# Kernel tuning notes

Measured on AMD Instinct MI355X. Metric: run time of the kernel, lower is better.

Reference implementation:

```python
import jax, jax.numpy as jnp
import numpy as np

NUM_HEADS = 8
LN_EPS = 1e-5


def layer_norm(x, g, b):
    m = jnp.mean(x, axis=-1, keepdims=True)
    v = jnp.mean((x - m) ** 2, axis=-1, keepdims=True)
    return (x - m) * jax.lax.rsqrt(v + LN_EPS) * g + b


def setup_inputs() -> dict:
    key = jax.random.key(0)
    B, Nq, Nk, D = 4, 2048, 2048, 256
    F = 4 * D
    ks = jax.random.split(key, 12)
    s = 0.02
    inp = {
        "q": jax.random.normal(ks[0], (B, Nq, D), jnp.float32),
        "x": jax.random.normal(ks[1], (B, Nk, D), jnp.float32),
        "Wq": jax.random.normal(ks[2], (D, D), jnp.float32) * s,
        "bq": jnp.zeros((D,), jnp.float32),
        "Wk": jax.random.normal(ks[3], (D, D), jnp.float32) * s,
        "bk": jnp.zeros((D,), jnp.float32),
        "Wv": jax.random.normal(ks[4], (D, D), jnp.float32) * s,
        "bv": jnp.zeros((D,), jnp.float32),
        "Wo": jax.random.normal(ks[5], (D, D), jnp.float32) * s,
        "bo": jnp.zeros((D,), jnp.float32),
        "Wm": jax.random.normal(ks[6], (D, F), jnp.float32) * s,
        "bm": jnp.zeros((F,), jnp.float32),
        "We": jax.random.normal(ks[7], (F, D), jnp.float32) * s,
        "be": jnp.zeros((D,), jnp.float32),
        "g0": jnp.ones((D,), jnp.float32),
        "b0": jnp.zeros((D,), jnp.float32),
        "g1": jnp.ones((D,), jnp.float32),
        "b1": jnp.zeros((D,), jnp.float32),
    }
    return inp


def reference(q, x, Wq, bq, Wk, bk, Wv, bv, Wo, bo, Wm, bm, We, be, g0, b0, g1, b1):
    B, Nq, D = q.shape
    H = NUM_HEADS
    dh = D // H
    scale = 1.0 / np.sqrt(dh).astype(np.float32)
    # projections, split into heads (split(dim_split,2)+cat(.,0) == head reshape)
    Q = (q @ Wq + bq).reshape(B, Nq, H, dh)
    K = (x @ Wk + bk).reshape(B, -1, H, dh)
    V = (x @ Wv + bv).reshape(B, -1, H, dh)
    A = jax.nn.softmax(jnp.einsum("bqhd,bkhd->bhqk", Q, K) * scale, axis=-1)
    # residual on the projected query (Q_ + A @ V_), merge heads
    O = (Q + jnp.einsum("bhqk,bkhd->bqhd", A, V)).reshape(B, Nq, D)
    O = layer_norm(O, g0, b0)
    O = O + jax.nn.relu(O @ Wo + bo)
    identity = O
    O = layer_norm(O, g1, b1)  # dropout p=0.0 is identity
    O = jax.nn.relu(O @ Wm + bm) @ We + be
    return O + identity
```

## Files before the change

### kernel.cpp

```cpp
#include <hip/hip_runtime.h>
#include <math.h>
#include <stdint.h>

typedef __attribute__((ext_vector_type(8))) __bf16 bf16x8;
typedef __attribute__((ext_vector_type(16))) float f32x16;

#define Z16 {0.f,0.f,0.f,0.f,0.f,0.f,0.f,0.f,0.f,0.f,0.f,0.f,0.f,0.f,0.f,0.f}

__device__ __forceinline__ unsigned short f2b(float f) {
  union { float f; uint32_t u; } v; v.f = f;
  uint32_t r = (v.u + 0x7FFFu + ((v.u >> 16) & 1u)) >> 16;
  return (unsigned short)r;
}
__device__ __forceinline__ float b2f(unsigned short u) {
  union { uint32_t u; float f; } v; v.u = ((uint32_t)u) << 16;
  return v.f;
}
__device__ __forceinline__ uint32_t pk2(float a, float b) {
  return (uint32_t)f2b(a) | ((uint32_t)f2b(b) << 16);
}
__device__ __forceinline__ uint32_t cvtpk(float lo, float hi) {
  uint32_t r;
  asm("v_cvt_pk_bf16_f32 %0, %1, %2" : "=v"(r) : "v"(lo), "v"(hi));
  return r;
}
__device__ __forceinline__ void glds16(const void* g, void* l) {
  __builtin_amdgcn_global_load_lds(
      (const __attribute__((address_space(1))) void*)g,
      (__attribute__((address_space(3))) void*)l, 16, 0, 0);
}
#define MFMA32(a, b, c) __builtin_amdgcn_mfma_f32_32x32x16_bf16(a, b, c, 0, 0, 0)

__global__ __launch_bounds__(256) void prep(
    const float* __restrict__ q, const float* __restrict__ x,
    unsigned short* __restrict__ qh, unsigned short* __restrict__ xh,
    const float* __restrict__ Wq, const float* __restrict__ Wk,
    const float* __restrict__ Wv, const float* __restrict__ Wo,
    const float* __restrict__ Wm, const float* __restrict__ We,
    unsigned short* __restrict__ WqT, unsigned short* __restrict__ WkvT,
    unsigned short* __restrict__ WoT, unsigned short* __restrict__ WmT,
    unsigned short* __restrict__ WeT,
    const float* __restrict__ bk, const float* __restrict__ bv,
    float* __restrict__ bkv) {
  __shared__ float T[64][68];
  const int bx = blockIdx.x, tid = threadIdx.x;
  if (bx < 2048) {
    const float* src = (bx < 1024) ? q : x;
    unsigned short* dst = (bx < 1024) ? qh : xh;
    const int i = (bx & 1023) * 256 + tid;
    float4 a = ((const float4*)src)[i * 2];
    float4 b = ((const float4*)src)[i * 2 + 1];
    uint4 o;
    o.x = cvtpk(a.x, a.y); o.y = cvtpk(a.z, a.w);
    o.z = cvtpk(b.x, b.y); o.w = cvtpk(b.z, b.w);
    ((uint4*)dst)[i] = o;
  } else if (bx < 2240) {
    int t = bx - 2048;
    const float* in; unsigned short* out; int ldin, ldout, kx, nx;
    if (t < 16)       { in = Wq; out = WqT;           ldin = 256;  ldout = 256;  kx = t & 3;  nx = t >> 2; }
    else if (t < 32)  { t -= 16;  in = Wk; out = WkvT;          ldin = 256;  ldout = 256;  kx = t & 3;  nx = t >> 2; }
    else if (t < 48)  { t -= 32;  in = Wv; out = WkvT + 65536;  ldin = 256;  ldout = 256;  kx = t & 3;  nx = t >> 2; }
    else if (t < 64)  { t -= 48;  in = Wo; out = WoT;           ldin = 256;  ldout = 256;  kx = t & 3;  nx = t >> 2; }
    else if (t < 128) { t -= 64;  in = Wm; out = WmT;           ldin = 1024; ldout = 256;  kx = t & 3;  nx = t >> 2; }
    else              { t -= 128; in = We; out = WeT;           ldin = 256;  ldout = 1024; kx = t & 15; nx = t >> 4; }
    const int k0 = kx * 64, n0 = nx * 64;
    const int r = tid >> 2, c16 = (tid & 3) * 16;
    #pragma unroll
    for (int i = 0; i < 4; ++i)
      *(float4*)&T[r][c16 + i * 4] =
          *(const float4*)&in[(size_t)(k0 + r) * ldin + n0 + c16 + i * 4];
    __syncthreads();
    const int n = tid >> 2, k16 = (tid & 3) * 16;
    uint32_t wb[8];
    #pragma unroll
    for (int p = 0; p < 8; ++p)
      wb[p] = cvtpk(T[k16 + 2 * p][n], T[k16 + 2 * p + 1][n]);
    uint4 o0, o1;
    o0.x = wb[0]; o0.y = wb[1]; o0.z = wb[2]; o0.w = wb[3];
    o1.x = wb[4]; o1.y = wb[5]; o1.z = wb[6]; o1.w = wb[7];
    *(uint4*)&out[(size_t)(n0 + n) * ldout + k0 + k16] = o0;
    *(uint4*)&out[(size_t)(n0 + n) * ldout + k0 + k16 + 8] = o1;
  } else {
    if (tid < 256) { bkv[tid] = bk[tid]; bkv[256 + tid] = bv[tid]; }
  }
}

__global__ __launch_bounds__(256, 2) void gemm_proj(
    const unsigned short* __restrict__ qh, const unsigned short* __restrict__ xh,
    const unsigned short* __restrict__ WqT, const unsigned short* __restrict__ WkvT,
    const float* __restrict__ bq, const float* __restrict__ bkv,
    unsigned short* __restrict__ Qb, unsigned short* __restrict__ Kb,
    unsigned short* __restrict__ Vt) {
  __shared__ __align__(16) unsigned short As[2 * 128 * 64];
  __shared__ __align__(16) unsigned short Bs[2 * 64 * 64];
  const int tid = threadIdx.x, lane = tid & 63, wid = tid >> 6;
  const int l31 = lane & 31, g2 = lane >> 5;
  const bool qmode = blockIdx.y < 4;
  const int m0 = blockIdx.x * 128;
  const int n0 = qmode ? blockIdx.y * 64 : (blockIdx.y - 4) * 64;
  const unsigned short* A = qmode ? qh : xh;
  const unsigned short* Bt = qmode ? WqT : WkvT;
  const float* bias = qmode ? bq : bkv;

  const char* srcA[4];
  const char* srcB[2];
  #pragma unroll
  for (int p = 0; p < 4; ++p) {
    int row = p * 32 + wid * 8 + (lane >> 3);
    srcA[p] = (const char*)A + ((size_t)(m0 + row) * 256) * 2 + (lane & 7) * 16;
  }
  #pragma unroll
  for (int p = 0; p < 2; ++p) {
    int row = p * 32 + wid * 8 + (lane >> 3);
    srcB[p] = (const char*)Bt + ((size_t)(n0 + row) * 256) * 2 + (lane & 7) * 16;
  }

  f32x16 acc0 = Z16, acc1 = Z16;

  #pragma unroll
  for (int p = 0; p < 4; ++p) { glds16(srcA[p], &As[p * 2048 + wid * 512]); srcA[p] += 128; }
  #pragma unroll
  for (int p = 0; p < 2; ++p) { glds16(srcB[p], &Bs[p * 2048 + wid * 512]); srcB[p] += 128; }
  __syncthreads();

  for (int t = 0; t < 4; ++t) {
    const int cur = t & 1, nxt = cur ^ 1;
    if (t + 1 < 4) {
      #pragma unroll
      for (int p = 0; p < 4; ++p) { glds16(srcA[p], &As[nxt * 8192 + p * 2048 + wid * 512]); srcA[p] += 128; }
      #pragma unroll
      for (int p = 0; p < 2; ++p) { glds16(srcB[p], &Bs[nxt * 4096 + p * 2048 + wid * 512]); srcB[p] += 128; }
    }
    const char* as = (const char*)As + cur * 16384;
    const char* bs = (const char*)Bs + cur * 8192;
    #pragma unroll
    for (int kc = 0; kc < 4; ++kc) {
      const int xo = kc * 32 + g2 * 16;
      bf16x8 af  = *(const bf16x8*)(as + (wid * 32 + l31) * 128 + xo);
      bf16x8 b0v = *(const bf16x8*)(bs + l31 * 128 + xo);
      bf16x8 b1v = *(const bf16x8*)(bs + (32 + l31) * 128 + xo);
      acc0 = MFMA32(af, b0v, acc0);
      acc1 = MFMA32(af, b1v, acc1);
    }
    __syncthreads();
  }

  const int bb = m0 >> 11;
  #pragma unroll
  for (int nb = 0; nb < 2; ++nb) {
    const f32x16& acc = nb ? acc1 : acc0;
    const int col = n0 + nb * 32 + l31;
    const float bs = bias[col];
    if (qmode) {
      #pragma unroll
      for (int r = 0; r < 16; ++r) {
        const int m = m0 + wid * 32 + (r & 3) + 8 * (r >> 2) + 4 * g2;
        Qb[(size_t)m * 256 + col] = f2b(acc[r] + bs);
      }
    } else if (n0 < 256) {
      #pragma unroll
      for (int r = 0; r < 16; ++r) {
        const int m = m0 + wid * 32 + (r & 3) + 8 * (r >> 2) + 4 * g2;
        Kb[(size_t)m * 256 + col] = f2b(acc[r] + bs);
      }
    } else {
      const int hv = (col - 256) >> 5, dv = (col - 256) & 31;
      unsigned short* vrow = Vt + ((size_t)(bb * 8 + hv) * 32 + dv) * 2048;
      #pragma unroll
      for (int tq = 0; tq < 4; ++tq) {
        const int ks = (m0 & 2047) + wid * 32 + 8 * tq + 4 * g2;
        uint2 wv;
        wv.x = pk2(acc[4 * tq + 0] + bs, acc[4 * tq + 1] + bs);
        wv.y = pk2(acc[4 * tq + 2] + bs, acc[4 * tq + 3] + bs);
        *(uint2*)(vrow + ks) = wv;
      }
    }
  }
}

template <int EPI>
__global__ __launch_bounds__(256, 2) void gemm_small(
    const unsigned short* __restrict__ A, int lda,
    const unsigned short* __restrict__ Bt, int ldb,
    const float* __restrict__ bias,
    const unsigned short* __restrict__ res, int ldr,
    void* __restrict__ Cout, int ldc, int K) {
  __shared__ __align__(16) unsigned short As[2 * 64 * 64];
  __shared__ __align__(16) unsigned short Bs[2 * 64 * 64];
  const int tid = threadIdx.x, lane = tid & 63, wid = tid >> 6;
  const int l31 = lane & 31, g2 = lane >> 5;
  const int m0 = blockIdx.x * 64, n0 = blockIdx.y * 64;
  const int wr = (wid >> 1) * 32, wc = (wid & 1) * 32;

  const char* srcA[2];
  const char* srcB[2];
  #pragma unroll
  for (int p = 0; p < 2; ++p) {
    int row = p * 32 + wid * 8 + (lane >> 3);
    srcA[p] = (const char*)A + ((size_t)(m0 + row) * lda) * 2 + (lane & 7) * 16;
    srcB[p] = (const char*)Bt + ((size_t)(n0 + row) * ldb) * 2 + (lane & 7) * 16;
  }

  f32x16 acc = Z16;
  const int nt = K >> 6;

  #pragma unroll
  for (int p = 0; p < 2; ++p) {
    glds16(srcA[p], &As[p * 2048 + wid * 512]); srcA[p] += 128;
    glds16(srcB[p], &Bs[p * 2048 + wid * 512]); srcB[p] += 128;
  }
  __syncthreads();

  for (int t = 0; t < nt; ++t) {
    const int cur = t & 1, nxt = cur ^ 1;
    if (t + 1 < nt) {
      #pragma unroll
      for (int p = 0; p < 2; ++p) {
        glds16(srcA[p], &As[nxt * 4096 + p * 2048 + wid * 512]); srcA[p] += 128;
        glds16(srcB[p], &Bs[nxt * 4096 + p * 2048 + wid * 512]); srcB[p] += 128;
      }
    }
    const char* as = (const char*)As + cur * 8192;
    const char* bs = (const char*)Bs + cur * 8192;
    #pragma unroll
    for (int kc = 0; kc < 4; ++kc) {
      const int xo = kc * 32 + g2 * 16;
      bf16x8 af = *(const bf16x8*)(as + (wr + l31) * 128 + xo);
      bf16x8 bf = *(const bf16x8*)(bs + (wc + l31) * 128 + xo);
      acc = MFMA32(af, bf, acc);
    }
    __syncthreads();
  }

  const int col = n0 + wc + l31;
  const float bs = bias[col];
  #pragma unroll
  for (int r = 0; r < 16; ++r) {
    const int m = m0 + wr + (r & 3) + 8 * (r >> 2) + 4 * g2;
    float v = acc[r] + bs;
    if (EPI == 1) v = fmaxf(v, 0.f);
    if (EPI == 1 || EPI == 3) v += b2f(res[(size_t)m * ldr + col]);
    if (EPI == 3)
      ((float*)Cout)[(size_t)m * ldc + col] = v;
    else
      ((unsigned short*)Cout)[(size_t)m * ldc + col] = f2b(v);
  }
}

__global__ __launch_bounds__(256, 2) void gemm_relu128(
    const unsigned short* __restrict__ A, int lda,
    const unsigned short* __restrict__ Bt, int ldb,
    const float* __restrict__ bias,
    unsigned short* __restrict__ Cout, int ldc, int K) {
  __shared__ __align__(16) unsigned short As[2 * 128 * 64];
  __shared__ __align__(16) unsigned short Bs[2 * 128 * 64];
  const int tid = threadIdx.x, lane = tid & 63, wid = tid >> 6;
  const int l31 = lane & 31, g2 = lane >> 5;
  const int m0 = blockIdx.x * 128, n0 = blockIdx.y * 128;
  const int wr = (wid >> 1) * 64, wc = (wid & 1) * 64;

  const char* srcA[4];
  const char* srcB[4];
  #pragma unroll
  for (int p = 0; p < 4; ++p) {
    int row = p * 32 + wid * 8 + (lane >> 3);
    srcA[p] = (const char*)A + ((size_t)(m0 + row) * lda) * 2 + (lane & 7) * 16;
    srcB[p] = (const char*)Bt + ((size_t)(n0 + row) * ldb) * 2 + (lane & 7) * 16;
  }

  f32x16 a00 = Z16, a01 = Z16, a10 = Z16, a11 = Z16;
  const int nt = K >> 6;

  #pragma unroll
  for (int p = 0; p < 4; ++p) {
    glds16(srcA[p], &As[p * 2048 + wid * 512]); srcA[p] += 128;
    glds16(srcB[p], &Bs[p * 2048 + wid * 512]); srcB[p] += 128;
  }
  __syncthreads();

  for (int t = 0; t < nt; ++t) {
    const int cur = t & 1, nxt = cur ^ 1;
    if (t + 1 < nt) {
      #pragma unroll
      for (int p = 0; p < 4; ++p) {
        glds16(srcA[p], &As[nxt * 8192 + p * 2048 + wid * 512]); srcA[p] += 128;
        glds16(srcB[p], &Bs[nxt * 8192 + p * 2048 + wid * 512]); srcB[p] += 128;
      }
    }
    const char* as = (const char*)As + cur * 16384;
    const char* bs = (const char*)Bs + cur * 16384;
    #pragma unroll
    for (int kc = 0; kc < 4; ++kc) {
      const int xo = kc * 32 + g2 * 16;
      bf16x8 af0 = *(const bf16x8*)(as + (wr + l31) * 128 + xo);
      bf16x8 af1 = *(const bf16x8*)(as + (wr + 32 + l31) * 128 + xo);
      bf16x8 bf0 = *(const bf16x8*)(bs + (wc + l31) * 128 + xo);
      bf16x8 bf1 = *(const bf16x8*)(bs + (wc + 32 + l31) * 128 + xo);
      a00 = MFMA32(af0, bf0, a00);
      a01 = MFMA32(af0, bf1, a01);
      a10 = MFMA32(af1, bf0, a10);
      a11 = MFMA32(af1, bf1, a11);
    }
    __syncthreads();
  }

  #pragma unroll
  for (int mf = 0; mf < 2; ++mf)
    #pragma unroll
    for (int nb = 0; nb < 2; ++nb) {
      const f32x16& acc = mf ? (nb ? a11 : a10) : (nb ? a01 : a00);
      const int col = n0 + wc + nb * 32 + l31;
      const float bs = bias[col];
      #pragma unroll
      for (int r = 0; r < 16; ++r) {
        const int m = m0 + wr + mf * 32 + (r & 3) + 8 * (r >> 2) + 4 * g2;
        Cout[(size_t)m * ldc + col] = f2b(fmaxf(acc[r] + bs, 0.f));
      }
    }
}

#define KLD 40
#define VLD2 136
__global__ __launch_bounds__(256, 4) void attn6(
    const unsigned short* __restrict__ Qg,
    const unsigned short* __restrict__ Kb,
    const unsigned short* __restrict__ Vt,
    unsigned short* __restrict__ Op0, unsigned short* __restrict__ Op1,
    unsigned short* __restrict__ Op2, unsigned short* __restrict__ Op3,
    unsigned short* __restrict__ lp) {
  __shared__ __align__(16) unsigned short Ks[128 * KLD];
  __shared__ __align__(16) unsigned short Vs[32 * VLD2];
  const int tid = threadIdx.x, lane = tid & 63, wid = tid >> 6;
  const int l31 = lane & 31, g2 = lane >> 5;
  const int w = (blockIdx.x >> 3) + (blockIdx.x & 7) * 256;
  const int b = w >> 9, h = (w >> 6) & 7, kv = (w >> 4) & 3, qt = w & 15;
  const int row0 = b * 2048 + qt * 128;
  const int qrow = row0 + wid * 32 + l31;
  const int kt0 = kv * 512;

  const float SCL2 = 0.17677669529663687f * 1.4426950408889634f;
  bf16x8 qf0, qf1;
  {
    const unsigned short* qp = Qg + (size_t)qrow * 256 + h * 32 + g2 * 8;
    #pragma unroll
    for (int dc = 0; dc < 2; ++dc) {
      ushort4 r0 = *(const ushort4*)(qp + dc * 16);
      ushort4 r1 = *(const ushort4*)(qp + dc * 16 + 4);
      union { unsigned short s[8]; bf16x8 v; } u;
      u.s[0] = f2b(b2f(r0.x) * SCL2); u.s[1] = f2b(b2f(r0.y) * SCL2);
      u.s[2] = f2b(b2f(r0.z) * SCL2); u.s[3] = f2b(b2f(r0.w) * SCL2);
      u.s[4] = f2b(b2f(r1.x) * SCL2); u.s[5] = f2b(b2f(r1.y) * SCL2);
      u.s[6] = f2b(b2f(r1.z) * SCL2); u.s[7] = f2b(b2f(r1.w) * SCL2);
      if (dc == 0) qf0 = u.v; else qf1 = u.v;
    }
  }

  const int ksr = tid >> 2, ksc = (tid & 3) * 8;
  const unsigned short* srcK = Kb + (size_t)(b * 2048 + kt0 + ksr) * 256 + h * 32 + ksc;
  const int vd = tid >> 3, vk = (tid & 7) * 8;
  const unsigned short* srcV = Vt + ((size_t)((b * 8 + h) * 32 + vd)) * 2048 + kt0 + vk;

  uint4 kreg0 = *(const uint4*)srcK;
  uint4 kreg1 = *(const uint4*)(srcK + 64 * 256);
  uint4 vreg0 = *(const uint4*)srcV;
  uint4 vreg1 = *(const uint4*)(srcV + 64);

  f32x16 oacc = Z16;
  float lr0 = 0.f, lr1 = 0.f;

  for (int kt = 0; kt < 512; kt += 128) {
    *(uint4*)&Ks[ksr * KLD + ksc] = kreg0;
    *(uint4*)&Ks[(64 + ksr) * KLD + ksc] = kreg1;
    *(uint4*)&Vs[vd * VLD2 + vk] = vreg0;
    *(uint4*)&Vs[vd * VLD2 + 64 + vk] = vreg1;
    __syncthreads();

    if (kt + 128 < 512) {
      srcK += 128 * 256;
      kreg0 = *(const uint4*)srcK;
      kreg1 = *(const uint4*)(srcK + 64 * 256);
      srcV += 128;
      vreg0 = *(const uint4*)srcV;
      vreg1 = *(const uint4*)(srcV + 64);
    }

    #pragma unroll
    for (int st = 0; st < 2; ++st) {
      const int kb0 = st * 64;
      f32x16 p0 = Z16, p1 = Z16;
      {
        bf16x8 k00 = *(const bf16x8*)&Ks[(kb0 + l31) * KLD + g2 * 8];
        bf16x8 k01 = *(const bf16x8*)&Ks[(kb0 + l31) * KLD + 16 + g2 * 8];
        bf16x8 k10 = *(const bf16x8*)&Ks[(kb0 + 32 + l31) * KLD + g2 * 8];
        bf16x8 k11 = *(const bf16x8*)&Ks[(kb0 + 32 + l31) * KLD + 16 + g2 * 8];
        p0 = MFMA32(k00, qf0, p0);
        p0 = MFMA32(k01, qf1, p0);
        p1 = MFMA32(k10, qf0, p1);
        p1 = MFMA32(k11, qf1, p1);
      }

      float s0 = 0.f, s1 = 0.f;
      #pragma unroll
      for (int i = 0; i < 16; ++i) { p0[i] = __builtin_amdgcn_exp2f(p0[i]); s0 += p0[i]; }
      #pragma unroll
      for (int i = 0; i < 16; ++i) { p1[i] = __builtin_amdgcn_exp2f(p1[i]); s1 += p1[i]; }
      lr0 += s0; lr1 += s1;

      #pragma unroll
      for (int rb = 0; rb < 2; ++rb) {
        const f32x16& pp = rb ? p1 : p0;
        #pragma unroll
        for (int c = 0; c < 2; ++c) {
          uint32_t A0 = cvtpk(pp[8 * c + 0], pp[8 * c + 1]);
          uint32_t A1 = cvtpk(pp[8 * c + 2], pp[8 * c + 3]);
          uint32_t B0 = cvtpk(pp[8 * c + 4], pp[8 * c + 5]);
          uint32_t B1 = cvtpk(pp[8 * c + 6], pp[8 * c + 7]);
          uint32_t pA0 = (uint32_t)__shfl_xor((int)A0, 32);
          uint32_t pB0 = (uint32_t)__shfl_xor((int)B0, 32);
          uint32_t pA1 = (uint32_t)__shfl_xor((int)A1, 32);
          uint32_t pB1 = (uint32_t)__shfl_xor((int)B1, 32);
          union { uint32_t u[4]; bf16x8 v; } fr;
          fr.u[0] = g2 ? pB0 : A0;
          fr.u[1] = g2 ? pB1 : A1;
          fr.u[2] = g2 ? B0 : pA0;
          fr.u[3] = g2 ? B1 : pA1;
          bf16x8 vf = *(const bf16x8*)&Vs[l31 * VLD2 + kb0 + rb * 32 + c * 16 + g2 * 8];
          oacc = MFMA32(vf, fr.v, oacc);
        }
      }
    }
    __syncthreads();
  }

  float lrun = lr0 + lr1;
  lrun += __shfl_xor(lrun, 32);
  unsigned short* op =
      (kv == 0 ? Op0 : kv == 1 ? Op1 : kv == 2 ? Op2 : Op3) +
      (size_t)qrow * 256 + h * 32;
  #pragma unroll
  for (int j = 0; j < 4; ++j) {
    uint2 wv;
    wv.x = cvtpk(oacc[4 * j + 0], oacc[4 * j + 1]);
    wv.y = cvtpk(oacc[4 * j + 2], oacc[4 * j + 3]);
    *(uint2*)(op + 8 * j + 4 * g2) = wv;
  }
  if (g2 == 0)
    lp[(((size_t)kv * 4 + b) * 8 + h) * 2048 + (qt * 128 + wid * 32 + l31)] = f2b(lrun);
}

__global__ __launch_bounds__(256) void combine_ln0(
    const unsigned short* __restrict__ Op0, const unsigned short* __restrict__ Op1,
    const unsigned short* __restrict__ Op2, const unsigned short* __restrict__ Op3,
    const unsigned short* __restrict__ lp,
    const unsigned short* __restrict__ Qb,
    const float* __restrict__ gw, const float* __restrict__ bw,
    unsigned short* __restrict__ O1n) {
  const int wid = threadIdx.x >> 6, lane = threadIdx.x & 63;
  const int row = blockIdx.x * 4 + wid;
  const int b = row >> 11, rr = row & 2047, hh = lane >> 3;
  float lsum = 0.f;
  #pragma unroll
  for (int s = 0; s < 4; ++s)
    lsum += b2f(lp[(((size_t)s * 4 + b) * 8 + hh) * 2048 + rr]);
  const float inv = 1.f / lsum;
  const size_t off = (size_t)row * 256 + lane * 4;
  ushort4 oa = *(const ushort4*)(Op0 + off);
  ushort4 ob = *(const ushort4*)(Op1 + off);
  ushort4 oc = *(const ushort4*)(Op2 + off);
  ushort4 od = *(const ushort4*)(Op3 + off);
  ushort4 qv = *(const ushort4*)(Qb + off);
  float x0 = b2f(qv.x) + (b2f(oa.x) + b2f(ob.x) + b2f(oc.x) + b2f(od.x)) * inv;
  float x1 = b2f(qv.y) + (b2f(oa.y) + b2f(ob.y) + b2f(oc.y) + b2f(od.y)) * inv;
  float x2 = b2f(qv.z) + (b2f(oa.z) + b2f(ob.z) + b2f(oc.z) + b2f(od.z)) * inv;
  float x3 = b2f(qv.w) + (b2f(oa.w) + b2f(ob.w) + b2f(oc.w) + b2f(od.w)) * inv;
  float s = x0 + x1 + x2 + x3;
  float sq = x0 * x0 + x1 * x1 + x2 * x2 + x3 * x3;
  #pragma unroll
  for (int off2 = 32; off2 >= 1; off2 >>= 1) {
    s += __shfl_xor(s, off2);
    sq += __shfl_xor(sq, off2);
  }
  const float mean = s * (1.f / 256.f);
  const float var = sq * (1.f / 256.f) - mean * mean;
  const float rstd = rsqrtf(var + 1e-5f);
  float4 gv = *(const float4*)&gw[lane * 4];
  float4 bv = *(const float4*)&bw[lane * 4];
  ushort4 o;
  o.x = f2b((x0 - mean) * rstd * gv.x + bv.x);
  o.y = f2b((x1 - mean) * rstd * gv.y + bv.y);
  o.z = f2b((x2 - mean) * rstd * gv.z + bv.z);
  o.w = f2b((x3 - mean) * rstd * gv.w + bv.w);
  *(ushort4*)(O1n + off) = o;
}

__global__ __launch_bounds__(256) void ln_k(
    const unsigned short* __restrict__ X, const float* __restrict__ gw,
    const float* __restrict__ bw, unsigned short* __restrict__ Y) {
  const int wid = threadIdx.x >> 6, lane = threadIdx.x & 63;
  const int row = blockIdx.x * 4 + wid;
  ushort4 xv = *(const ushort4*)(X + (size_t)row * 256 + lane * 4);
  float x0 = b2f(xv.x), x1 = b2f(xv.y), x2 = b2f(xv.z), x3 = b2f(xv.w);
  float s = x0 + x1 + x2 + x3;
  float sq = x0 * x0 + x1 * x1 + x2 * x2 + x3 * x3;
  #pragma unroll
  for (int off = 32; off >= 1; off >>= 1) {
    s += __shfl_xor(s, off);
    sq += __shfl_xor(sq, off);
  }
  const float mean = s * (1.f / 256.f);
  const float var = sq * (1.f / 256.f) - mean * mean;
  const float rstd = rsqrtf(var + 1e-5f);
  float4 gv = *(const float4*)&gw[lane * 4];
  float4 bv = *(const float4*)&bw[lane * 4];
  ushort4 o;
  o.x = f2b((x0 - mean) * rstd * gv.x + bv.x);
  o.y = f2b((x1 - mean) * rstd * gv.y + bv.y);
  o.z = f2b((x2 - mean) * rstd * gv.z + bv.z);
  o.w = f2b((x3 - mean) * rstd * gv.w + bv.w);
  *(ushort4*)(Y + (size_t)row * 256 + lane * 4) = o;
}

extern "C" void kernel_launch(void* const* d_in, const int* in_sizes, int n_in,
                              void* d_out, int out_size, void* d_ws, size_t ws_size,
                              hipStream_t stream) {
  (void)in_sizes; (void)n_in; (void)out_size; (void)ws_size;
  const float* q = (const float*)d_in[0];
  const float* x = (const float*)d_in[1];
  const float* Wq = (const float*)d_in[2];
  const float* bq = (const float*)d_in[3];
  const float* Wk = (const float*)d_in[4];
  const float* bk = (const float*)d_in[5];
  const float* Wv = (const float*)d_in[6];
  const float* bv = (const float*)d_in[7];
  const float* Wo = (const float*)d_in[8];
  const float* bo = (const float*)d_in[9];
  const float* Wm = (const float*)d_in[10];
  const float* bm = (const float*)d_in[11];
  const float* We = (const float*)d_in[12];
  const float* be = (const float*)d_in[13];
  const float* g0 = (const float*)d_in[14];
  const float* b0 = (const float*)d_in[15];
  const float* g1 = (const float*)d_in[16];
  const float* b1 = (const float*)d_in[17];
  float* out = (float*)d_out;

  uint8_t* ws = (uint8_t*)d_ws;
  unsigned short* WoT  = (unsigned short*)(ws + 0);
  unsigned short* WmT  = (unsigned short*)(ws + 131072);
  unsigned short* WeT  = (unsigned short*)(ws + 655360);
  float*          bkv  = (float*)(ws + 1179648);
  unsigned short* WqT  = (unsigned short*)(ws + 1181696);
  unsigned short* WkvT = (unsigned short*)(ws + 1312768);
  unsigned short* qh   = (unsigned short*)(ws + 1576960);
  unsigned short* xh   = (unsigned short*)(ws + 5771264);
  unsigned short* Qb   = (unsigned short*)(ws + 9965568);
  unsigned short* Kb   = (unsigned short*)(ws + 14159872);
  unsigned short* Vt   = (unsigned short*)(ws + 18354176);
  unsigned short* lp   = (unsigned short*)(ws + 22548480);
  unsigned short* Op0 = qh;
  unsigned short* Op1 = xh;
  unsigned short* Op2 = (unsigned short*)d_out;
  unsigned short* Op3 = (unsigned short*)d_out + 2097152;
  unsigned short* O1n = (unsigned short*)(ws + 14159872);
  unsigned short* O2  = (unsigned short*)(ws + 1576960);
  unsigned short* O2n = (unsigned short*)(ws + 5771264);
  unsigned short* Mb  = (unsigned short*)(ws + 14159872);

  prep<<<2241, 256, 0, stream>>>(q, x, qh, xh, Wq, Wk, Wv, Wo, Wm, We,
                                 WqT, WkvT, WoT, WmT, WeT, bk, bv, bkv);

  gemm_proj<<<dim3(64, 12), 256, 0, stream>>>(qh, xh, WqT, WkvT, bq, bkv, Qb, Kb, Vt);

  attn6<<<2048, 256, 0, stream>>>(Qb, Kb, Vt, Op0, Op1, Op2, Op3, lp);
  combine_ln0<<<2048, 256, 0, stream>>>(Op0, Op1, Op2, Op3, lp, Qb, g0, b0, O1n);

  gemm_small<1><<<dim3(128, 4), 256, 0, stream>>>(O1n, 256, WoT, 256, bo, O1n, 256, O2, 256, 256);
  ln_k<<<2048, 256, 0, stream>>>(O2, g1, b1, O2n);

  gemm_relu128<<<dim3(64, 8), 256, 0, stream>>>(O2n, 256, WmT, 256, bm, Mb, 1024, 256);
  gemm_small<3><<<dim3(128, 4), 256, 0, stream>>>(Mb, 1024, WeT, 1024, be, O2, 256, out, 256, 1024);
}
```

Before: 107.9 us.

## Fuse attention combine+LN0 into Wo GEMM and LN1 into Wm GEMM

Replaces the separate combine_ln0, gemm_small<1>, ln_k and gemm_relu128 launches with two fused kernels. wo_fused merges the split-KV partial outputs, adds the Q residual, applies layernorm in shared memory and then runs the Wo GEMM with relu and residual. wm_fused applies layernorm to a 64-row tile in LDS and runs the Wm GEMM with register-staged double buffering of the weights. This removes two launches and the global round-trips of the normalized intermediates, but each Wo block recomputes the combine and layernorm for its rows (four-fold redundancy across the column blocks), and the Wm path also recomputes layernorm once per column block.

```diff
diff --git a/kernel.cpp b/kernel.cpp
--- a/kernel.cpp
+++ b/kernel.cpp
@@ -30,6 +30,8 @@
       (__attribute__((address_space(3))) void*)l, 16, 0, 0);
 }
 #define MFMA32(a, b, c) __builtin_amdgcn_mfma_f32_32x32x16_bf16(a, b, c, 0, 0, 0)
+
+union U8 { uint4 u; unsigned short s[8]; };
 
 __global__ __launch_bounds__(256) void prep(
     const float* __restrict__ q, const float* __restrict__ x,
@@ -247,78 +249,6 @@
   }
 }
 
-__global__ __launch_bounds__(256, 2) void gemm_relu128(
-    const unsigned short* __restrict__ A, int lda,
-    const unsigned short* __restrict__ Bt, int ldb,
-    const float* __restrict__ bias,
-    unsigned short* __restrict__ Cout, int ldc, int K) {
-  __shared__ __align__(16) unsigned short As[2 * 128 * 64];
-  __shared__ __align__(16) unsigned short Bs[2 * 128 * 64];
-  const int tid = threadIdx.x, lane = tid & 63, wid = tid >> 6;
-  const int l31 = lane & 31, g2 = lane >> 5;
-  const int m0 = blockIdx.x * 128, n0 = blockIdx.y * 128;
-  const int wr = (wid >> 1) * 64, wc = (wid & 1) * 64;
-
-  const char* srcA[4];
-  const char* srcB[4];
-  #pragma unroll
-  for (int p = 0; p < 4; ++p) {
-    int row = p * 32 + wid * 8 + (lane >> 3);
-    srcA[p] = (const char*)A + ((size_t)(m0 + row) * lda) * 2 + (lane & 7) * 16;
-    srcB[p] = (const char*)Bt + ((size_t)(n0 + row) * ldb) * 2 + (lane & 7) * 16;
-  }
-
-  f32x16 a00 = Z16, a01 = Z16, a10 = Z16, a11 = Z16;
-  const int nt = K >> 6;
-
-  #pragma unroll
-  for (int p = 0; p < 4; ++p) {
-    glds16(srcA[p], &As[p * 2048 + wid * 512]); srcA[p] += 128;
-    glds16(srcB[p], &Bs[p * 2048 + wid * 512]); srcB[p] += 128;
-  }
-  __syncthreads();
-
-  for (int t = 0; t < nt; ++t) {
-    const int cur = t & 1, nxt = cur ^ 1;
-    if (t + 1 < nt) {
-      #pragma unroll
-      for (int p = 0; p < 4; ++p) {
-        glds16(srcA[p], &As[nxt * 8192 + p * 2048 + wid * 512]); srcA[p] += 128;
-        glds16(srcB[p], &Bs[nxt * 8192 + p * 2048 + wid * 512]); srcB[p] += 128;
-      }
-    }
-    const char* as = (const char*)As + cur * 16384;
-    const char* bs = (const char*)Bs + cur * 16384;
-    #pragma unroll
-    for (int kc = 0; kc < 4; ++kc) {
-      const int xo = kc * 32 + g2 * 16;
-      bf16x8 af0 = *(const bf16x8*)(as + (wr + l31) * 128 + xo);
-      bf16x8 af1 = *(const bf16x8*)(as + (wr + 32 + l31) * 128 + xo);
-      bf16x8 bf0 = *(const bf16x8*)(bs + (wc + l31) * 128 + xo);
-      bf16x8 bf1 = *(const bf16x8*)(bs + (wc + 32 + l31) * 128 + xo);
-      a00 = MFMA32(af0, bf0, a00);
-      a01 = MFMA32(af0, bf1, a01);
-      a10 = MFMA32(af1, bf0, a10);
-      a11 = MFMA32(af1, bf1, a11);
-    }
-    __syncthreads();
-  }
-
-  #pragma unroll
-  for (int mf = 0; mf < 2; ++mf)
-    #pragma unroll
-    for (int nb = 0; nb < 2; ++nb) {
-      const f32x16& acc = mf ? (nb ? a11 : a10) : (nb ? a01 : a00);
-      const int col = n0 + wc + nb * 32 + l31;
-      const float bs = bias[col];
-      #pragma unroll
-      for (int r = 0; r < 16; ++r) {
-        const int m = m0 + wr + mf * 32 + (r & 3) + 8 * (r >> 2) + 4 * g2;
-        Cout[(size_t)m * ldc + col] = f2b(fmaxf(acc[r] + bs, 0.f));
-      }
-    }
-}
-
 #define KLD 40
 #define VLD2 136
 __global__ __launch_bounds__(256, 4) void attn6(
@@ -448,76 +378,205 @@
     lp[(((size_t)kv * 4 + b) * 8 + h) * 2048 + (qt * 128 + wid * 32 + l31)] = f2b(lrun);
 }
 
-__global__ __launch_bounds__(256) void combine_ln0(
+#define ALD 264
+__global__ __launch_bounds__(256, 2) void wo_fused(
     const unsigned short* __restrict__ Op0, const unsigned short* __restrict__ Op1,
     const unsigned short* __restrict__ Op2, const unsigned short* __restrict__ Op3,
-    const unsigned short* __restrict__ lp,
-    const unsigned short* __restrict__ Qb,
-    const float* __restrict__ gw, const float* __restrict__ bw,
-    unsigned short* __restrict__ O1n) {
-  const int wid = threadIdx.x >> 6, lane = threadIdx.x & 63;
-  const int row = blockIdx.x * 4 + wid;
-  const int b = row >> 11, rr = row & 2047, hh = lane >> 3;
-  float lsum = 0.f;
-  #pragma unroll
-  for (int s = 0; s < 4; ++s)
-    lsum += b2f(lp[(((size_t)s * 4 + b) * 8 + hh) * 2048 + rr]);
-  const float inv = 1.f / lsum;
-  const size_t off = (size_t)row * 256 + lane * 4;
-  ushort4 oa = *(const ushort4*)(Op0 + off);
-  ushort4 ob = *(const ushort4*)(Op1 + off);
-  ushort4 oc = *(const ushort4*)(Op2 + off);
-  ushort4 od = *(const ushort4*)(Op3 + off);
-  ushort4 qv = *(const ushort4*)(Qb + off);
-  float x0 = b2f(qv.x) + (b2f(oa.x) + b2f(ob.x) + b2f(oc.x) + b2f(od.x)) * inv;
-  float x1 = b2f(qv.y) + (b2f(oa.y) + b2f(ob.y) + b2f(oc.y) + b2f(od.y)) * inv;
-  float x2 = b2f(qv.z) + (b2f(oa.z) + b2f(ob.z) + b2f(oc.z) + b2f(od.z)) * inv;
-  float x3 = b2f(qv.w) + (b2f(oa.w) + b2f(ob.w) + b2f(oc.w) + b2f(od.w)) * inv;
-  float s = x0 + x1 + x2 + x3;
-  float sq = x0 * x0 + x1 * x1 + x2 * x2 + x3 * x3;
-  #pragma unroll
-  for (int off2 = 32; off2 >= 1; off2 >>= 1) {
-    s += __shfl_xor(s, off2);
-    sq += __shfl_xor(sq, off2);
-  }
-  const float mean = s * (1.f / 256.f);
-  const float var = sq * (1.f / 256.f) - mean * mean;
-  const float rstd = rsqrtf(var + 1e-5f);
-  float4 gv = *(const float4*)&gw[lane * 4];
-  float4 bv = *(const float4*)&bw[lane * 4];
-  ushort4 o;
-  o.x = f2b((x0 - mean) * rstd * gv.x + bv.x);
-  o.y = f2b((x1 - mean) * rstd * gv.y + bv.y);
-  o.z = f2b((x2 - mean) * rstd * gv.z + bv.z);
-  o.w = f2b((x3 - mean) * rstd * gv.w + bv.w);
-  *(ushort4*)(O1n + off) = o;
-}
-
-__global__ __launch_bounds__(256) void ln_k(
-    const unsigned short* __restrict__ X, const float* __restrict__ gw,
-    const float* __restrict__ bw, unsigned short* __restrict__ Y) {
-  const int wid = threadIdx.x >> 6, lane = threadIdx.x & 63;
-  const int row = blockIdx.x * 4 + wid;
-  ushort4 xv = *(const ushort4*)(X + (size_t)row * 256 + lane * 4);
-  float x0 = b2f(xv.x), x1 = b2f(xv.y), x2 = b2f(xv.z), x3 = b2f(xv.w);
-  float s = x0 + x1 + x2 + x3;
-  float sq = x0 * x0 + x1 * x1 + x2 * x2 + x3 * x3;
-  #pragma unroll
-  for (int off = 32; off >= 1; off >>= 1) {
-    s += __shfl_xor(s, off);
-    sq += __shfl_xor(sq, off);
-  }
-  const float mean = s * (1.f / 256.f);
-  const float var = sq * (1.f / 256.f) - mean * mean;
-  const float rstd = rsqrtf(var + 1e-5f);
-  float4 gv = *(const float4*)&gw[lane * 4];
-  float4 bv = *(const float4*)&bw[lane * 4];
-  ushort4 o;
-  o.x = f2b((x0 - mean) * rstd * gv.x + bv.x);
-  o.y = f2b((x1 - mean) * rstd * gv.y + bv.y);
-  o.z = f2b((x2 - mean) * rstd * gv.z + bv.z);
-  o.w = f2b((x3 - mean) * rstd * gv.w + bv.w);
-  *(ushort4*)(Y + (size_t)row * 256 + lane * 4) = o;
+    const unsigned short* __restrict__ lp, const unsigned short* __restrict__ Qb,
+    const float* __restrict__ g0, const float* __restrict__ b0,
+    const unsigned short* __restrict__ WoT, const float* __restrict__ bo,
+    unsigned short* __restrict__ O2out) {
+  __shared__ __align__(16) unsigned short Aln[64 * ALD];
+  __shared__ __align__(16) unsigned short Bs[64 * ALD];
+  const int tid = threadIdx.x, lane = tid & 63, wid = tid >> 6;
+  const int l31 = lane & 31, g2 = lane >> 5;
+  const int n0 = blockIdx.x * 64, m0 = blockIdx.y * 64;
+  const int wr = (wid >> 1) * 32, wc = (wid & 1) * 32;
+  const int row = tid >> 2, cq = (tid & 3) * 64;
+
+  {
+    const unsigned short* src = WoT + (size_t)(n0 + row) * 256 + cq;
+    #pragma unroll
+    for (int j = 0; j < 8; ++j) {
+      uint4 v = *(const uint4*)(src + j * 8);
+      *(uint4*)&Bs[row * ALD + cq + j * 8] = v;
+    }
+  }
+
+  {
+    const int grow = m0 + row;
+    const int bb = grow >> 11, rr = grow & 2047;
+    const int hh0 = cq >> 5;
+    float ls0 = 0.f, ls1 = 0.f;
+    #pragma unroll
+    for (int s = 0; s < 4; ++s) {
+      ls0 += b2f(lp[(((size_t)s * 4 + bb) * 8 + hh0) * 2048 + rr]);
+      ls1 += b2f(lp[(((size_t)s * 4 + bb) * 8 + hh0 + 1) * 2048 + rr]);
+    }
+    const float inv0 = 1.f / ls0, inv1 = 1.f / ls1;
+    const size_t base = (size_t)grow * 256 + cq;
+    float sa = 0.f, sqa = 0.f;
+    #pragma unroll
+    for (int j = 0; j < 8; ++j) {
+      U8 o0, o1, o2, o3, qv, wv;
+      o0.u = *(const uint4*)(Op0 + base + j * 8);
+      o1.u = *(const uint4*)(Op1 + base + j * 8);
+      o2.u = *(const uint4*)(Op2 + base + j * 8);
+      o3.u = *(const uint4*)(Op3 + base + j * 8);
+      qv.u = *(const uint4*)(Qb + base + j * 8);
+      const float inv = (j < 4) ? inv0 : inv1;
+      #pragma unroll
+      for (int e = 0; e < 8; ++e) {
+        float xx = b2f(qv.s[e]) +
+                   (b2f(o0.s[e]) + b2f(o1.s[e]) + b2f(o2.s[e]) + b2f(o3.s[e])) * inv;
+        sa += xx; sqa += xx * xx;
+        wv.s[e] = f2b(xx);
+      }
+      *(uint4*)&Aln[row * ALD + cq + j * 8] = wv.u;
+    }
+    sa += __shfl_xor(sa, 1);  sa += __shfl_xor(sa, 2);
+    sqa += __shfl_xor(sqa, 1); sqa += __shfl_xor(sqa, 2);
+    const float mean = sa * (1.f / 256.f);
+    const float var = sqa * (1.f / 256.f) - mean * mean;
+    const float rstd = rsqrtf(var + 1e-5f);
+    #pragma unroll
+    for (int j = 0; j < 8; ++j) {
+      U8 wv; wv.u = *(uint4*)&Aln[row * ALD + cq + j * 8];
+      float4 ga = *(const float4*)&g0[cq + j * 8];
+      float4 gb = *(const float4*)&g0[cq + j * 8 + 4];
+      float4 ba = *(const float4*)&b0[cq + j * 8];
+      float4 bbv = *(const float4*)&b0[cq + j * 8 + 4];
+      wv.s[0] = f2b((b2f(wv.s[0]) - mean) * rstd * ga.x + ba.x);
+      wv.s[1] = f2b((b2f(wv.s[1]) - mean) * rstd * ga.y + ba.y);
+      wv.s[2] = f2b((b2f(wv.s[2]) - mean) * rstd * ga.z + ba.z);
+      wv.s[3] = f2b((b2f(wv.s[3]) - mean) * rstd * ga.w + ba.w);
+      wv.s[4] = f2b((b2f(wv.s[4]) - mean) * rstd * gb.x + bbv.x);
+      wv.s[5] = f2b((b2f(wv.s[5]) - mean) * rstd * gb.y + bbv.y);
+      wv.s[6] = f2b((b2f(wv.s[6]) - mean) * rstd * gb.z + bbv.z);
+      wv.s[7] = f2b((b2f(wv.s[7]) - mean) * rstd * gb.w + bbv.w);
+      *(uint4*)&Aln[row * ALD + cq + j * 8] = wv.u;
+    }
+  }
+  __syncthreads();
+
+  f32x16 acc = Z16;
+  #pragma unroll
+  for (int ks = 0; ks < 16; ++ks) {
+    const int xo = ks * 32 + g2 * 16;
+    bf16x8 af = *(const bf16x8*)((const char*)Aln + (wr + l31) * (ALD * 2) + xo);
+    bf16x8 bf = *(const bf16x8*)((const char*)Bs + (wc + l31) * (ALD * 2) + xo);
+    acc = MFMA32(af, bf, acc);
+  }
+
+  const int col = n0 + wc + l31;
+  const float bs = bo[col];
+  #pragma unroll
+  for (int r = 0; r < 16; ++r) {
+    const int m = m0 + wr + (r & 3) + 8 * (r >> 2) + 4 * g2;
+    float v = fmaxf(acc[r] + bs, 0.f);
+    v += b2f(Aln[(m - m0) * ALD + col]);
+    O2out[(size_t)m * 256 + col] = f2b(v);
+  }
+}
+
+#define BLD 72
+__global__ __launch_bounds__(256, 2) void wm_fused(
+    const unsigned short* __restrict__ O2in,
+    const float* __restrict__ g1, const float* __restrict__ b1,
+    const unsigned short* __restrict__ WmT, const float* __restrict__ bm,
+    unsigned short* __restrict__ Mb) {
+  __shared__ __align__(16) unsigned short Aln[64 * ALD];
+  __shared__ __align__(16) unsigned short Bs[2 * 128 * BLD];
+  const int tid = threadIdx.x, lane = tid & 63, wid = tid >> 6;
+  const int l31 = lane & 31, g2 = lane >> 5;
+  const int n0 = blockIdx.x * 128, m0 = blockIdx.y * 64;
+  const int wr = (wid >> 1) * 32, wc = (wid & 1) * 64;
+
+  const int brow = tid >> 1, bkq = (tid & 1) * 32;
+  const unsigned short* srcB = WmT + (size_t)(n0 + brow) * 256 + bkq;
+  uint4 breg[4];
+  #pragma unroll
+  for (int j = 0; j < 4; ++j) breg[j] = *(const uint4*)(srcB + j * 8);
+
+  {
+    const int row = tid >> 2, cq = (tid & 3) * 64;
+    const int grow = m0 + row;
+    const size_t base = (size_t)grow * 256 + cq;
+    float sa = 0.f, sqa = 0.f;
+    #pragma unroll
+    for (int j = 0; j < 8; ++j) {
+      U8 wv; wv.u = *(const uint4*)(O2in + base + j * 8);
+      #pragma unroll
+      for (int e = 0; e < 8; ++e) {
+        float xx = b2f(wv.s[e]);
+        sa += xx; sqa += xx * xx;
+      }
+      *(uint4*)&Aln[row * ALD + cq + j * 8] = wv.u;
+    }
+    sa += __shfl_xor(sa, 1);  sa += __shfl_xor(sa, 2);
+    sqa += __shfl_xor(sqa, 1); sqa += __shfl_xor(sqa, 2);
+    const float mean = sa * (1.f / 256.f);
+    const float var = sqa * (1.f / 256.f) - mean * mean;
+    const float rstd = rsqrtf(var + 1e-5f);
+    #pragma unroll
+    for (int j = 0; j < 8; ++j) {
+      U8 wv; wv.u = *(uint4*)&Aln[row * ALD + cq + j * 8];
+      float4 ga = *(const float4*)&g1[cq + j * 8];
+      float4 gb = *(const float4*)&g1[cq + j * 8 + 4];
+      float4 ba = *(const float4*)&b1[cq + j * 8];
+      float4 bbv = *(const float4*)&b1[cq + j * 8 + 4];
+      wv.s[0] = f2b((b2f(wv.s[0]) - mean) * rstd * ga.x + ba.x);
+      wv.s[1] = f2b((b2f(wv.s[1]) - mean) * rstd * ga.y + ba.y);
+      wv.s[2] = f2b((b2f(wv.s[2]) - mean) * rstd * ga.z + ba.z);
+      wv.s[3] = f2b((b2f(wv.s[3]) - mean) * rstd * ga.w + ba.w);
+      wv.s[4] = f2b((b2f(wv.s[4]) - mean) * rstd * gb.x + bbv.x);
+      wv.s[5] = f2b((b2f(wv.s[5]) - mean) * rstd * gb.y + bbv.y);
+      wv.s[6] = f2b((b2f(wv.s[6]) - mean) * rstd * gb.z + bbv.z);
+      wv.s[7] = f2b((b2f(wv.s[7]) - mean) * rstd * gb.w + bbv.w);
+      *(uint4*)&Aln[row * ALD + cq + j * 8] = wv.u;
+    }
+  }
+  #pragma unroll
+  for (int j = 0; j < 4; ++j)
+    *(uint4*)&Bs[brow * BLD + bkq + j * 8] = breg[j];
+  __syncthreads();
+
+  f32x16 a0 = Z16, a1 = Z16;
+  for (int t = 0; t < 4; ++t) {
+    if (t < 3) {
+      #pragma unroll
+      for (int j = 0; j < 4; ++j)
+        breg[j] = *(const uint4*)(srcB + (t + 1) * 64 + j * 8);
+    }
+    const char* bsc = (const char*)Bs + (t & 1) * (128 * BLD * 2);
+    #pragma unroll
+    for (int kc = 0; kc < 4; ++kc) {
+      const int ks = t * 4 + kc;
+      bf16x8 af = *(const bf16x8*)((const char*)Aln + (wr + l31) * (ALD * 2) + ks * 32 + g2 * 16);
+      bf16x8 b0f = *(const bf16x8*)(bsc + (wc + l31) * (BLD * 2) + kc * 32 + g2 * 16);
+      bf16x8 b1f = *(const bf16x8*)(bsc + (wc + 32 + l31) * (BLD * 2) + kc * 32 + g2 * 16);
+      a0 = MFMA32(af, b0f, a0);
+      a1 = MFMA32(af, b1f, a1);
+    }
+    if (t < 3) {
+      #pragma unroll
+      for (int j = 0; j < 4; ++j)
+        *(uint4*)&Bs[((t + 1) & 1) * (128 * BLD) + brow * BLD + bkq + j * 8] = breg[j];
+    }
+    __syncthreads();
+  }
+
+  #pragma unroll
+  for (int nb = 0; nb < 2; ++nb) {
+    const f32x16& acc = nb ? a1 : a0;
+    const int col = n0 + wc + nb * 32 + l31;
+    const float bs = bm[col];
+    #pragma unroll
+    for (int r = 0; r < 16; ++r) {
+      const int m = m0 + wr + (r & 3) + 8 * (r >> 2) + 4 * g2;
+      Mb[(size_t)m * 1024 + col] = f2b(fmaxf(acc[r] + bs, 0.f));
+    }
+  }
 }
 
 extern "C" void kernel_launch(void* const* d_in, const int* in_sizes, int n_in,
@@ -561,10 +620,8 @@
   unsigned short* Op1 = xh;
   unsigned short* Op2 = (unsigned short*)d_out;
   unsigned short* Op3 = (unsigned short*)d_out + 2097152;
-  unsigned short* O1n = (unsigned short*)(ws + 14159872);
-  unsigned short* O2  = (unsigned short*)(ws + 1576960);
-  unsigned short* O2n = (unsigned short*)(ws + 5771264);
-  unsigned short* Mb  = (unsigned short*)(ws + 14159872);
+  unsigned short* O2  = (unsigned short*)(ws + 18354176);
+  unsigned short* Mb  = (unsigned short*)(ws + 1576960);
 
   prep<<<2241, 256, 0, stream>>>(q, x, qh, xh, Wq, Wk, Wv, Wo, Wm, We,
                                  WqT, WkvT, WoT, WmT, WeT, bk, bv, bkv);
@@ -572,11 +629,11 @@
   gemm_proj<<<dim3(64, 12), 256, 0, stream>>>(qh, xh, WqT, WkvT, bq, bkv, Qb, Kb, Vt);
 
   attn6<<<2048, 256, 0, stream>>>(Qb, Kb, Vt, Op0, Op1, Op2, Op3, lp);
-  combine_ln0<<<2048, 256, 0, stream>>>(Op0, Op1, Op2, Op3, lp, Qb, g0, b0, O1n);
-
-  gemm_small<1><<<dim3(128, 4), 256, 0, stream>>>(O1n, 256, WoT, 256, bo, O1n, 256, O2, 256, 256);
-  ln_k<<<2048, 256, 0, stream>>>(O2, g1, b1, O2n);
-
-  gemm_relu128<<<dim3(64, 8), 256, 0, stream>>>(O2n, 256, WmT, 256, bm, Mb, 1024, 256);
+
+  wo_fused<<<dim3(4, 128), 256, 0, stream>>>(Op0, Op1, Op2, Op3, lp, Qb,
+                                             g0, b0, WoT, bo, O2);
+
+  wm_fused<<<dim3(8, 128), 256, 0, stream>>>(O2, g1, b1, WmT, bm, Mb);
+
   gemm_small<3><<<dim3(128, 4), 256, 0, stream>>>(Mb, 1024, WeT, 1024, be, O2, 256, out, 256, 1024);
 }
```

Measured after the change: 181.7 us. 1.68x slower.
